# Optimization experiments

Measured on AMD Instinct MI355X. Metric: run time of the kernel, lower is better.

The kernel has to match this reference:

```python
import jax, jax.numpy as jnp
import numpy as np


def setup_inputs() -> dict:
    key = jax.random.key(0)
    B, T, FFT, HOP = 16, 2048, 1024, 256
    n_bins = FFT // 2 + 1  # 513
    stfts = jax.random.normal(key, (B, T, n_bins, 2), dtype=jnp.float32)
    return {"stfts": stfts, "frame_length": FFT, "frame_step": HOP, "fft_length": FFT}


def reference(stfts, frame_length, frame_step, fft_length):
    # --- precomputed constants (built in the layer's build()) ---
    n = jnp.arange(fft_length, dtype=jnp.float32)
    angles = (2.0 * np.pi / fft_length) * (n[:, None] * n[None, :])  # [fft, fft]
    idft_cos = jnp.cos(angles)
    idft_sin = jnp.sin(angles)
    # periodic Hann window
    t = jnp.arange(frame_length, dtype=jnp.float32)
    window = 0.5 - 0.5 * jnp.cos(2.0 * np.pi * t / frame_length)
    hop_ratio = frame_step / frame_length
    normalization = np.sqrt(1.0 / (1.0 - hop_ratio + 1e-8))
    syn_window = window / np.float32(normalization)
    if fft_length > frame_length:
        syn_window = jnp.pad(syn_window, (0, fft_length - frame_length))

    # --- forward ---
    real_part = stfts[..., 0]  # [B, T, n_bins]
    imag_part = stfts[..., 1]
    if fft_length % 2 == 0:
        mirror_real = real_part[:, :, 1:-1]
        mirror_imag = imag_part[:, :, 1:-1]
    else:
        mirror_real = real_part[:, :, 1:]
        mirror_imag = imag_part[:, :, 1:]
    full_real = jnp.concatenate([real_part, mirror_real[:, :, ::-1]], axis=-1)   # [B, T, fft]
    full_imag = jnp.concatenate([imag_part, -mirror_imag[:, :, ::-1]], axis=-1)  # [B, T, fft]

    # explicit IDFT via dense matmul (transpose_b in TF; matrices are symmetric)
    time_real = jnp.einsum('btf,nf->btn', full_real, idft_cos)
    time_real = time_real - jnp.einsum('btf,nf->btn', full_imag, idft_sin)
    time_real = time_real / jnp.float32(fft_length)

    windowed = (time_real * syn_window[None, None, :])[:, :, :frame_length]  # [B, T, frame_length]

    # overlap-and-add
    B, T, L = windowed.shape
    out_len = (T - 1) * frame_step + frame_length
    idx = jnp.arange(T)[:, None] * frame_step + jnp.arange(L)[None, :]  # [T, L]
    out = jnp.zeros((B, out_len), dtype=windowed.dtype).at[:, idx].add(windowed)
    return out
```

## Files before the change

### kernel.cpp

```cpp
#include <hip/hip_runtime.h>
#include <hip/hip_bf16.h>
#include <math.h>


#define BATCH  16
#define TFR    2048
#define NB     513
#define HOP    256
#define OUTLEN 525056
#define RROWS  2051
#define PBR    2054
#define FSTR   1040
#define KTOT   (4 * FSTR)
#define BK     32
#define NKT    (KTOT / BK)
#define KVAL   1026
#define MTB    33
#define MTOT   (BATCH * MTB)
#define TOTROW (BATCH * PBR + 128)
#define CHPR   (FSTR / 8)

typedef __attribute__((ext_vector_type(4))) float f32x4;
typedef __attribute__((ext_vector_type(8))) short bf16x8;

__device__ __forceinline__ void load_lds16(const void* g, void* l)
{
    __builtin_amdgcn_global_load_lds((const __attribute__((address_space(1))) void*)g,
                                     (__attribute__((address_space(3))) void*)l,
                                     16, 0, 0);
}

#define STEP 6.13592315e-3f

__global__ __launch_bounds__(256)
void build_B(__hip_bfloat16* __restrict__ Bg)
{
    __shared__ float cosT[1024];
    __shared__ float sinT[1024];
    const int j = blockIdx.x;
    for (int i = threadIdx.x; i < 1024; i += 256) {
        float s, c;
        sincosf((float)i * STEP, &s, &c);
        cosT[i] = c; sinT[i] = s;
    }
    __syncthreads();

    for (int k = threadIdx.x; k < KTOT; k += 256) {
        const int d  = k / FSTR;
        const int kk = k - d * FSTR;
        float val = 0.f;
        if (kk < KVAL) {
            const int   f   = kk >> 1;
            const int   n   = 768 - 256 * d + j;
            const float syn = (0.5f - 0.5f * cosT[n]) * 0.8660254f * (1.0f / 1024.0f);
            const int   idx = (n * f) & 1023;
            if ((kk & 1) == 0) {
                const float wr = (f == 0 || f == 512) ? 1.f : 2.f;
                val = wr * cosT[idx] * syn;
            } else {
                val = -2.f * sinT[idx] * syn;
            }
        }
        Bg[(size_t)j * KTOT + k] = __float2bfloat16(val);
    }
}

__global__ __launch_bounds__(256)
void convert_A(const float* __restrict__ A, __hip_bfloat16* __restrict__ Ab)
{
    const int idx = blockIdx.x * 256 + threadIdx.x;
    if (idx >= TOTROW * CHPR) return;
    const int row = idx / CHPR;
    const int c8  = (idx - row * CHPR) * 8;

    const int b  = row / PBR;
    const int rr = row - b * PBR;
    const bool valid = (b < BATCH) && (rr >= 3) && (rr < 3 + TFR);

    union { bf16x8 v; __hip_bfloat162 h[4]; } u;
    if (valid) {
        const int t = rr - 3;
        const float* src = A + (size_t)(b * TFR + t) * KVAL + c8;
        #pragma unroll
        for (int j = 0; j < 8; j += 2) {
            float2 p = make_float2(0.f, 0.f);
            if (c8 + j < KVAL)
                p = *reinterpret_cast<const float2*>(src + j);
            u.h[j >> 1] = __float22bfloat162_rn(p);
        }
    } else {
        #pragma unroll
        for (int j = 0; j < 4; ++j) u.h[j] = __float22bfloat162_rn(make_float2(0.f, 0.f));
    }
    *reinterpret_cast<bf16x8*>(Ab + (size_t)row * FSTR + c8) = u.v;
}

__global__ __launch_bounds__(64)
void istft_gemm5(const __hip_bfloat16* __restrict__ Ab,
                 const __hip_bfloat16* __restrict__ Bg,
                 float* __restrict__ out)
{
    __shared__ __hip_bfloat16 Asl[2][64 * BK];
    __shared__ __hip_bfloat16 Bsl[2][64 * BK];

    const int lane = threadIdx.x;

    const int wg   = blockIdx.x;
    const int xcd  = wg & 7;
    const int slot = wg >> 3;
    const int mtg  = xcd * 66 + (slot >> 2);
    const int nt   = slot & 3;

    const int b  = mtg / MTB;
    const int rt = (mtg - b * MTB) * 64;
    const int n0 = nt * 64;

    const int srow = lane >> 2;
    const int scol = (lane & 3) * 8;
    const __hip_bfloat16* gA = Ab + ((size_t)b * PBR + rt + srow) * FSTR + scol;
    const __hip_bfloat16* gB = Bg + (size_t)(n0 + srow) * KTOT + scol;

    const int fr = lane & 15;
    const int fk = (lane >> 4) * 8;

    f32x4 acc[4][4] = {};

#define STAGE(buf, kt)                                                          \
    {                                                                           \
        const int _ko = (kt) * BK;                                              \
        _Pragma("unroll")                                                       \
        for (int _i = 0; _i < 4; ++_i) {                                        \
            load_lds16(gA + (size_t)_i * 16 * FSTR + _ko,                       \
                       &Asl[buf][_i * 512 + lane * 8]);                         \
            load_lds16(gB + (size_t)_i * 16 * KTOT + _ko,                       \
                       &Bsl[buf][_i * 512 + lane * 8]);                         \
        }                                                                       \
    }

    STAGE(0, 0)
    STAGE(1, 1)

    for (int kt = 0; kt < NKT; ++kt) {
        if (kt + 1 < NKT) { asm volatile("s_waitcnt vmcnt(8)" ::: "memory"); }
        else              { asm volatile("s_waitcnt vmcnt(0)" ::: "memory"); }
        __builtin_amdgcn_sched_barrier(0);

        const int buf = kt & 1;
        bf16x8 a[4], bv[4];
        #pragma unroll
        for (int mi = 0; mi < 4; ++mi)
            a[mi] = *reinterpret_cast<const bf16x8*>(&Asl[buf][(mi * 16 + fr) * BK + fk]);
        #pragma unroll
        for (int ni = 0; ni < 4; ++ni)
            bv[ni] = *reinterpret_cast<const bf16x8*>(&Bsl[buf][(ni * 16 + fr) * BK + fk]);

        asm volatile("s_waitcnt lgkmcnt(0)" ::: "memory");
        __builtin_amdgcn_sched_barrier(0);

        if (kt + 2 < NKT) STAGE(buf, kt + 2)

        #pragma unroll
        for (int mi = 0; mi < 4; ++mi)
            #pragma unroll
            for (int ni = 0; ni < 4; ++ni)
                acc[mi][ni] = __builtin_amdgcn_mfma_f32_16x16x32_bf16(
                    a[mi], bv[ni], acc[mi][ni], 0, 0, 0);
    }
#undef STAGE

    const int cr = (lane >> 4) * 4;
    const int cc = lane & 15;
    #pragma unroll
    for (int mi = 0; mi < 4; ++mi) {
        #pragma unroll
        for (int ni = 0; ni < 4; ++ni) {
            const int col = n0 + ni * 16 + cc;
            #pragma unroll
            for (int j = 0; j < 4; ++j) {
                const int r = rt + mi * 16 + cr + j;
                if (r < RROWS)
                    out[(size_t)b * OUTLEN + (size_t)r * 256 + col] = acc[mi][ni][j];
            }
        }
    }
}

extern "C" void kernel_launch(void* const* d_in, const int* in_sizes, int n_in,
                              void* d_out, int out_size, void* d_ws, size_t ws_size,
                              hipStream_t stream)
{
    const float* A = reinterpret_cast<const float*>(d_in[0]);
    float* out = reinterpret_cast<float*>(d_out);

    const size_t abBytes = (size_t)TOTROW * FSTR * sizeof(__hip_bfloat16);
    __hip_bfloat16* Ab = reinterpret_cast<__hip_bfloat16*>(d_ws);
    __hip_bfloat16* Bg = reinterpret_cast<__hip_bfloat16*>((char*)d_ws + abBytes);

    build_B<<<dim3(256), dim3(256), 0, stream>>>(Bg);

    const int nChunks = TOTROW * CHPR;
    convert_A<<<dim3((nChunks + 255) / 256), dim3(256), 0, stream>>>(A, Ab);

    istft_gemm5<<<dim3(MTOT * 4), dim3(64), 0, stream>>>(Ab, Bg, out);
}
```

Measured before the change: 222.6 us.

## Split GEMM K dimension across four waves with LDS reduction

The ISTFT GEMM previously ran one wave per workgroup, with K concatenated over the four overlap offsets. It now uses four waves per workgroup, each handling one overlap offset (d) with its own K=1056 slice. The partial tiles are reduced through LDS atomics and written out as float4 stores. The A matrix layout drops the padded shifted-row scheme in favour of clamped row indexing. The per-wave pipeline drops from double buffering to single buffering with a full vmcnt(0) wait, which may expose memory latency, and the reduction adds sync and atomic cost.

Result: slower. 300.7 us (+35.1%).

```diff
diff --git a/kernel.cpp b/kernel.cpp
--- a/kernel.cpp
+++ b/kernel.cpp
@@ -5,20 +5,15 @@
 
 #define BATCH  16
 #define TFR    2048
-#define NB     513
 #define HOP    256
 #define OUTLEN 525056
 #define RROWS  2051
-#define PBR    2054
-#define FSTR   1040
-#define KTOT   (4 * FSTR)
+#define KPAD   1056
+#define KVAL   1026
 #define BK     32
-#define NKT    (KTOT / BK)
-#define KVAL   1026
+#define NKT    (KPAD / BK)
 #define MTB    33
-#define MTOT   (BATCH * MTB)
-#define TOTROW (BATCH * PBR + 128)
-#define CHPR   (FSTR / 8)
+#define CHPR   (KPAD / 8)
 
 typedef __attribute__((ext_vector_type(4))) float f32x4;
 typedef __attribute__((ext_vector_type(8))) short bf16x8;
@@ -37,7 +32,10 @@
 {
     __shared__ float cosT[1024];
     __shared__ float sinT[1024];
-    const int j = blockIdx.x;
+    const int g = blockIdx.x;
+    const int d = g >> 8;
+    const int j = g & 255;
+    const int n = (3 - d) * 256 + j;
     for (int i = threadIdx.x; i < 1024; i += 256) {
         float s, c;
         sincosf((float)i * STEP, &s, &c);
@@ -45,23 +43,20 @@
     }
     __syncthreads();
 
-    for (int k = threadIdx.x; k < KTOT; k += 256) {
-        const int d  = k / FSTR;
-        const int kk = k - d * FSTR;
+    const float syn = (0.5f - 0.5f * cosT[n]) * 0.8660254f * (1.0f / 1024.0f);
+    for (int k = threadIdx.x; k < KPAD; k += 256) {
         float val = 0.f;
-        if (kk < KVAL) {
-            const int   f   = kk >> 1;
-            const int   n   = 768 - 256 * d + j;
-            const float syn = (0.5f - 0.5f * cosT[n]) * 0.8660254f * (1.0f / 1024.0f);
-            const int   idx = (n * f) & 1023;
-            if ((kk & 1) == 0) {
+        if (k < KVAL) {
+            const int f   = k >> 1;
+            const int idx = (n * f) & 1023;
+            if ((k & 1) == 0) {
                 const float wr = (f == 0 || f == 512) ? 1.f : 2.f;
                 val = wr * cosT[idx] * syn;
             } else {
                 val = -2.f * sinT[idx] * syn;
             }
         }
-        Bg[(size_t)j * KTOT + k] = __float2bfloat16(val);
+        Bg[(size_t)g * KPAD + k] = __float2bfloat16(val);
     }
 }
 
@@ -69,95 +64,90 @@
 void convert_A(const float* __restrict__ A, __hip_bfloat16* __restrict__ Ab)
 {
     const int idx = blockIdx.x * 256 + threadIdx.x;
-    if (idx >= TOTROW * CHPR) return;
-    const int row = idx / CHPR;
-    const int c8  = (idx - row * CHPR) * 8;
-
-    const int b  = row / PBR;
-    const int rr = row - b * PBR;
-    const bool valid = (b < BATCH) && (rr >= 3) && (rr < 3 + TFR);
-
+    if (idx >= BATCH * TFR * CHPR) return;
+    const int m  = idx / CHPR;
+    const int k8 = (idx - m * CHPR) * 8;
+
+    const float* src = A + (size_t)m * KVAL + k8;
     union { bf16x8 v; __hip_bfloat162 h[4]; } u;
-    if (valid) {
-        const int t = rr - 3;
-        const float* src = A + (size_t)(b * TFR + t) * KVAL + c8;
-        #pragma unroll
-        for (int j = 0; j < 8; j += 2) {
-            float2 p = make_float2(0.f, 0.f);
-            if (c8 + j < KVAL)
-                p = *reinterpret_cast<const float2*>(src + j);
-            u.h[j >> 1] = __float22bfloat162_rn(p);
-        }
-    } else {
-        #pragma unroll
-        for (int j = 0; j < 4; ++j) u.h[j] = __float22bfloat162_rn(make_float2(0.f, 0.f));
-    }
-    *reinterpret_cast<bf16x8*>(Ab + (size_t)row * FSTR + c8) = u.v;
-}
-
-__global__ __launch_bounds__(64)
-void istft_gemm5(const __hip_bfloat16* __restrict__ Ab,
+    #pragma unroll
+    for (int j = 0; j < 8; j += 2) {
+        float2 p = make_float2(0.f, 0.f);
+        if (k8 + j < KVAL)
+            p = *reinterpret_cast<const float2*>(src + j);
+        u.h[j >> 1] = __float22bfloat162_rn(p);
+    }
+    *reinterpret_cast<bf16x8*>(Ab + (size_t)m * KPAD + k8) = u.v;
+}
+
+__global__ __launch_bounds__(256)
+void istft_gemm6(const __hip_bfloat16* __restrict__ Ab,
                  const __hip_bfloat16* __restrict__ Bg,
                  float* __restrict__ out)
 {
-    __shared__ __hip_bfloat16 Asl[2][64 * BK];
-    __shared__ __hip_bfloat16 Bsl[2][64 * BK];
-
-    const int lane = threadIdx.x;
+    __shared__ __align__(16) char pool[32768];
+
+    const int tid  = threadIdx.x;
+    const int lane = tid & 63;
+    const int d    = tid >> 6;
 
     const int wg   = blockIdx.x;
     const int xcd  = wg & 7;
     const int slot = wg >> 3;
     const int mtg  = xcd * 66 + (slot >> 2);
     const int nt   = slot & 3;
-
-    const int b  = mtg / MTB;
-    const int rt = (mtg - b * MTB) * 64;
-    const int n0 = nt * 64;
+    const int b    = mtg / MTB;
+    const int rt   = (mtg - b * MTB) * 64;
+    const int n0   = nt * 64;
+
+    __hip_bfloat16* Asl = (__hip_bfloat16*)(pool + d * 8192);
+    __hip_bfloat16* Bsl = (__hip_bfloat16*)(pool + d * 8192 + 4096);
 
     const int srow = lane >> 2;
     const int scol = (lane & 3) * 8;
-    const __hip_bfloat16* gA = Ab + ((size_t)b * PBR + rt + srow) * FSTR + scol;
-    const __hip_bfloat16* gB = Bg + (size_t)(n0 + srow) * KTOT + scol;
+
+    const __hip_bfloat16* gA[4];
+    const __hip_bfloat16* gB[4];
+    #pragma unroll
+    for (int i = 0; i < 4; ++i) {
+        int t = rt - 3 + d + i * 16 + srow;
+        t = t < 0 ? 0 : (t > TFR - 1 ? TFR - 1 : t);
+        gA[i] = Ab + ((size_t)b * TFR + t) * KPAD + scol;
+        gB[i] = Bg + (size_t)(d * 256 + n0 + i * 16 + srow) * KPAD + scol;
+    }
 
     const int fr = lane & 15;
     const int fk = (lane >> 4) * 8;
 
     f32x4 acc[4][4] = {};
 
-#define STAGE(buf, kt)                                                          \
-    {                                                                           \
-        const int _ko = (kt) * BK;                                              \
-        _Pragma("unroll")                                                       \
-        for (int _i = 0; _i < 4; ++_i) {                                        \
-            load_lds16(gA + (size_t)_i * 16 * FSTR + _ko,                       \
-                       &Asl[buf][_i * 512 + lane * 8]);                         \
-            load_lds16(gB + (size_t)_i * 16 * KTOT + _ko,                       \
-                       &Bsl[buf][_i * 512 + lane * 8]);                         \
-        }                                                                       \
-    }
-
-    STAGE(0, 0)
-    STAGE(1, 1)
-
+#define STAGE(kt)                                                              \
+    {                                                                          \
+        const int _ko = (kt) * BK;                                             \
+        _Pragma("unroll")                                                      \
+        for (int _i = 0; _i < 4; ++_i) {                                       \
+            load_lds16(gA[_i] + _ko, Asl + _i * 512 + lane * 8);               \
+            load_lds16(gB[_i] + _ko, Bsl + _i * 512 + lane * 8);               \
+        }                                                                      \
+    }
+
+    STAGE(0)
     for (int kt = 0; kt < NKT; ++kt) {
-        if (kt + 1 < NKT) { asm volatile("s_waitcnt vmcnt(8)" ::: "memory"); }
-        else              { asm volatile("s_waitcnt vmcnt(0)" ::: "memory"); }
+        asm volatile("s_waitcnt vmcnt(0)" ::: "memory");
         __builtin_amdgcn_sched_barrier(0);
 
-        const int buf = kt & 1;
         bf16x8 a[4], bv[4];
         #pragma unroll
         for (int mi = 0; mi < 4; ++mi)
-            a[mi] = *reinterpret_cast<const bf16x8*>(&Asl[buf][(mi * 16 + fr) * BK + fk]);
+            a[mi] = *reinterpret_cast<const bf16x8*>(&Asl[(mi * 16 + fr) * BK + fk]);
         #pragma unroll
         for (int ni = 0; ni < 4; ++ni)
-            bv[ni] = *reinterpret_cast<const bf16x8*>(&Bsl[buf][(ni * 16 + fr) * BK + fk]);
+            bv[ni] = *reinterpret_cast<const bf16x8*>(&Bsl[(ni * 16 + fr) * BK + fk]);
 
         asm volatile("s_waitcnt lgkmcnt(0)" ::: "memory");
         __builtin_amdgcn_sched_barrier(0);
 
-        if (kt + 2 < NKT) STAGE(buf, kt + 2)
+        if (kt + 1 < NKT) STAGE(kt + 1)
 
         #pragma unroll
         for (int mi = 0; mi < 4; ++mi)
@@ -168,19 +158,49 @@
     }
 #undef STAGE
 
+    float* red = (float*)pool;
     const int cr = (lane >> 4) * 4;
     const int cc = lane & 15;
-    #pragma unroll
-    for (int mi = 0; mi < 4; ++mi) {
-        #pragma unroll
-        for (int ni = 0; ni < 4; ++ni) {
-            const int col = n0 + ni * 16 + cc;
+
+    __syncthreads();
+
+    if (d == 0) {
+        #pragma unroll
+        for (int mi = 0; mi < 4; ++mi)
             #pragma unroll
-            for (int j = 0; j < 4; ++j) {
-                const int r = rt + mi * 16 + cr + j;
-                if (r < RROWS)
-                    out[(size_t)b * OUTLEN + (size_t)r * 256 + col] = acc[mi][ni][j];
-            }
+            for (int ni = 0; ni < 4; ++ni)
+                #pragma unroll
+                for (int j = 0; j < 4; ++j) {
+                    const int row = mi * 16 + cr + j;
+                    const int t   = rt + row - 3;
+                    const float v = (t >= 0 && t < TFR) ? acc[mi][ni][j] : 0.f;
+                    red[row * 64 + ni * 16 + cc] = v;
+                }
+    }
+    __syncthreads();
+    if (d != 0) {
+        #pragma unroll
+        for (int mi = 0; mi < 4; ++mi)
+            #pragma unroll
+            for (int ni = 0; ni < 4; ++ni)
+                #pragma unroll
+                for (int j = 0; j < 4; ++j) {
+                    const int row = mi * 16 + cr + j;
+                    const int t   = rt + row - 3 + d;
+                    if (t >= 0 && t < TFR)
+                        atomicAdd(&red[row * 64 + ni * 16 + cc], acc[mi][ni][j]);
+                }
+    }
+    __syncthreads();
+
+    float* og = out + (size_t)b * OUTLEN;
+    for (int idx = tid; idx < 64 * 16; idx += 256) {
+        const int row = idx >> 4;
+        const int c4  = (idx & 15) * 4;
+        const int r   = rt + row;
+        if (r < RROWS) {
+            const float4 v = *reinterpret_cast<const float4*>(&red[row * 64 + c4]);
+            *reinterpret_cast<float4*>(&og[(size_t)r * 256 + n0 + c4]) = v;
         }
     }
 }
@@ -192,14 +212,14 @@
     const float* A = reinterpret_cast<const float*>(d_in[0]);
     float* out = reinterpret_cast<float*>(d_out);
 
-    const size_t abBytes = (size_t)TOTROW * FSTR * sizeof(__hip_bfloat16);
+    const size_t abBytes = (size_t)BATCH * TFR * KPAD * sizeof(__hip_bfloat16);
     __hip_bfloat16* Ab = reinterpret_cast<__hip_bfloat16*>(d_ws);
     __hip_bfloat16* Bg = reinterpret_cast<__hip_bfloat16*>((char*)d_ws + abBytes);
 
-    build_B<<<dim3(256), dim3(256), 0, stream>>>(Bg);
-
-    const int nChunks = TOTROW * CHPR;
+    build_B<<<dim3(1024), dim3(256), 0, stream>>>(Bg);
+
+    const int nChunks = BATCH * TFR * CHPR;
     convert_A<<<dim3((nChunks + 255) / 256), dim3(256), 0, stream>>>(A, Ab);
 
-    istft_gemm5<<<dim3(MTOT * 4), dim3(64), 0, stream>>>(Ab, Bg, out);
-}
+    istft_gemm6<<<dim3(BATCH * MTB * 4), dim3(256), 0, stream>>>(Ab, Bg, out);
+}
```
